# Kernel optimization log

Hardware: AMD Instinct MI355X
Metric: run time of the kernel (lower is better)

Reference implementation:

```python
import jax, jax.numpy as jnp
import numpy as np

N_NODES = 50000


def setup_inputs() -> dict:
    key = jax.random.key(0)
    k1, k2, k3, k4, k5 = jax.random.split(key, 5)
    E = 1600000
    features = jax.random.normal(k1, (N_NODES, 256), dtype=jnp.float32)
    weight = jax.random.normal(k2, (256, 64), dtype=jnp.float32) * (1.0 / np.sqrt(256))
    edge_row = jax.random.randint(k3, (E,), 0, N_NODES, dtype=jnp.int64 if jax.config.jax_enable_x64 else jnp.int32)
    edge_col = jax.random.randint(k4, (E,), 0, N_NODES, dtype=jnp.int64 if jax.config.jax_enable_x64 else jnp.int32)
    edge_weight = jax.random.uniform(k5, (E,), dtype=jnp.float32)
    return {
        "features": features,
        "weight": weight,
        "edge_row": edge_row,
        "edge_col": edge_col,
        "edge_weight": edge_weight,
        "active": 1,
    }


def reference(features, weight, edge_row, edge_col, edge_weight, active):
    # support = features @ W  -- dense projection [N, out]
    support = features @ weight
    # output = spmm(adj, support): gather source rows, scale by edge weight,
    # scatter-add into destination rows (COO SpMM).
    msgs = support[edge_col] * edge_weight[:, None]           # [E, out]
    output = jax.ops.segment_sum(msgs, edge_row, num_segments=N_NODES)  # [N, out]
    if active:
        output = jnp.tanh(output)
    return output
```

## Files before the change

kernel.cpp:

```cpp
#include <hip/hip_runtime.h>
#include <hip/hip_fp16.h>
#include <math.h>

#define N_NODES 50000
#define IN_F 256
#define OUT_F 64
#define NBUCK 512
#define BROWS 98
#define CHUNK 6272
#define NI4   (CHUNK / 4)
#define CAPB 3584

typedef unsigned int uint;
typedef __attribute__((ext_vector_type(8))) short short8v;
typedef __attribute__((ext_vector_type(4))) short short4v;
typedef __attribute__((ext_vector_type(4))) float f32x4;


__device__ __forceinline__ short bf16_trunc(float f) {
    return (short)(__float_as_uint(f) >> 16);
}
__device__ __forceinline__ float bf16_tof(short s) {
    return __uint_as_float(((uint)(unsigned short)s) << 16);
}
__device__ __forceinline__ short bf16_rne(float f) {
    uint u = __float_as_uint(f);
    uint r = u + 0x7FFF + ((u >> 16) & 1);
    return (short)(r >> 16);
}

__global__ __launch_bounds__(256) void wprep_kernel(const float* __restrict__ W,
                                                    short* __restrict__ Whi,
                                                    short* __restrict__ Wlo,
                                                    int* __restrict__ gcnt) {
    const int t = threadIdx.x;
    const int k0 = blockIdx.x * 32;
    if (blockIdx.x == 0) {
        for (int i = t; i < NBUCK; i += 256) gcnt[i] = 0;
    }

    __shared__ float buf[32][65];
    for (int i = t; i < 32 * 64; i += 256) {
        int kk = i >> 6, c = i & 63;
        buf[kk][c] = W[(k0 + kk) * 64 + c];
    }
    __syncthreads();
    {
        int c = t & 63, g = t >> 6;
        short8v vh, vl;
        for (int j = 0; j < 8; ++j) {
            float f = buf[g * 8 + j][c];
            short h = bf16_trunc(f);
            vh[j] = h;
            vl[j] = bf16_rne(f - bf16_tof(h));
        }
        *(short8v*)&Whi[c * IN_F + k0 + g * 8] = vh;
        *(short8v*)&Wlo[c * IN_F + k0 + g * 8] = vl;
    }
}

__global__ __launch_bounds__(256) void gemm_kernel(const float* __restrict__ feat,
                                                   const short* __restrict__ Whi,
                                                   const short* __restrict__ Wlo,
                                                   __half* __restrict__ sup) {
    __shared__ short lds[15360];
    short* As_hi = lds;
    short* As_lo = lds + 5120;
    short* Bs_hi = lds + 10240;
    short* Bs_lo = lds + 12800;

    const int t = threadIdx.x;
    const int row0 = blockIdx.x * 128;
    const int l = t & 63;
    const int lr = l & 15;
    const int lk = (l >> 4) * 8;
    const int wrow = (t >> 6) * 32;

    const int ar = t >> 1, aq = t & 1;
    int gr = row0 + ar; if (gr >= N_NODES) gr = N_NODES - 1;
    const float4* asrc = (const float4*)(feat + (size_t)gr * IN_F);
    const int bc = t >> 2, bp = t & 3;

    f32x4 acc[2][4];
#pragma unroll
    for (int m = 0; m < 2; ++m)
#pragma unroll
        for (int nn = 0; nn < 4; ++nn) acc[m][nn] = (f32x4)(0.f);

    for (int ch = 0; ch < 8; ++ch) {
        float4 av[4];
#pragma unroll
        for (int i = 0; i < 4; ++i) av[i] = asrc[ch * 8 + aq * 4 + i];
        short8v bh = *(const short8v*)(Whi + bc * IN_F + ch * 32 + bp * 8);
        short8v bl = *(const short8v*)(Wlo + bc * IN_F + ch * 32 + bp * 8);

        __syncthreads();
#pragma unroll
        for (int i = 0; i < 4; ++i) {
            float fx[4] = {av[i].x, av[i].y, av[i].z, av[i].w};
            short4v h4, l4;
#pragma unroll
            for (int j = 0; j < 4; ++j) {
                short h = bf16_trunc(fx[j]);
                h4[j] = h;
                l4[j] = bf16_rne(fx[j] - bf16_tof(h));
            }
            *(short4v*)&As_hi[ar * 40 + aq * 16 + i * 4] = h4;
            *(short4v*)&As_lo[ar * 40 + aq * 16 + i * 4] = l4;
        }
        *(short8v*)&Bs_hi[bc * 40 + bp * 8] = bh;
        *(short8v*)&Bs_lo[bc * 40 + bp * 8] = bl;
        __syncthreads();

        short8v ah[2], al[2], wh[4], wl[4];
#pragma unroll
        for (int m = 0; m < 2; ++m) {
            ah[m] = *(short8v*)&As_hi[(wrow + m * 16 + lr) * 40 + lk];
            al[m] = *(short8v*)&As_lo[(wrow + m * 16 + lr) * 40 + lk];
        }
#pragma unroll
        for (int nn = 0; nn < 4; ++nn) {
            wh[nn] = *(short8v*)&Bs_hi[(nn * 16 + lr) * 40 + lk];
            wl[nn] = *(short8v*)&Bs_lo[(nn * 16 + lr) * 40 + lk];
        }
#pragma unroll
        for (int m = 0; m < 2; ++m)
#pragma unroll
            for (int nn = 0; nn < 4; ++nn) {
                acc[m][nn] = __builtin_amdgcn_mfma_f32_16x16x32_bf16(ah[m], wh[nn], acc[m][nn], 0, 0, 0);
                acc[m][nn] = __builtin_amdgcn_mfma_f32_16x16x32_bf16(ah[m], wl[nn], acc[m][nn], 0, 0, 0);
                acc[m][nn] = __builtin_amdgcn_mfma_f32_16x16x32_bf16(al[m], wh[nn], acc[m][nn], 0, 0, 0);
            }
    }

    __syncthreads();
    short* sup_s = lds;
#pragma unroll
    for (int m = 0; m < 2; ++m) {
        int rr = wrow + m * 16 + (l >> 4) * 4;
#pragma unroll
        for (int nn = 0; nn < 4; ++nn) {
            int cc = nn * 16 + lr;
#pragma unroll
            for (int j = 0; j < 4; ++j) {
                __half h = __float2half(acc[m][nn][j]);
                sup_s[(rr + j) * 64 + cc] = *(short*)&h;
            }
        }
    }
    __syncthreads();
    {
        int r = t >> 1, sg = (t & 1) * 32;
        int grow = row0 + r;
        if (grow < N_NODES) {
            const uint4* s4 = (const uint4*)&sup_s[r * 64 + sg];
            uint4* d4 = (uint4*)(sup + (size_t)grow * OUT_F + sg);
            d4[0] = s4[0];
            d4[1] = s4[1];
            d4[2] = s4[2];
            d4[3] = s4[3];
        }
    }
}

__global__ __launch_bounds__(1024) void bin_kernel(const int* __restrict__ erow,
                                                   const int* __restrict__ ecol,
                                                   const float* __restrict__ ew,
                                                   int* __restrict__ gcnt,
                                                   int2* __restrict__ ecw, int E) {
    __shared__ int   h[NBUCK];
    __shared__ uint  pkst[CHUNK];
    __shared__ float wst[CHUNK];
    const int t = threadIdx.x;
    const int base = blockIdx.x * CHUNK;

    for (int i = t; i < NBUCK; i += 1024) h[i] = 0;
    __syncthreads();

    for (int i4 = t; i4 < NI4; i4 += 1024) {
        const int e4 = base + 4 * i4;
        if (e4 + 3 < E) {
            int4   r4 = *(const int4*)(erow + e4);
            int4   c4 = *(const int4*)(ecol + e4);
            float4 w4 = *(const float4*)(ew + e4);
            pkst[4 * i4 + 0] = ((uint)r4.x << 16) | (uint)c4.x;
            pkst[4 * i4 + 1] = ((uint)r4.y << 16) | (uint)c4.y;
            pkst[4 * i4 + 2] = ((uint)r4.z << 16) | (uint)c4.z;
            pkst[4 * i4 + 3] = ((uint)r4.w << 16) | (uint)c4.w;
            *(float4*)(wst + 4 * i4) = w4;
            atomicAdd(&h[(uint)r4.x / BROWS], 1);
            atomicAdd(&h[(uint)r4.y / BROWS], 1);
            atomicAdd(&h[(uint)r4.z / BROWS], 1);
            atomicAdd(&h[(uint)r4.w / BROWS], 1);
        } else {
            for (int k = 0; k < 4; ++k) {
                int e = e4 + k;
                if (e < E) {
                    int row = erow[e];
                    pkst[4 * i4 + k] = ((uint)row << 16) | (uint)ecol[e];
                    wst[4 * i4 + k] = ew[e];
                    atomicAdd(&h[(uint)row / BROWS], 1);
                }
            }
        }
    }
    __syncthreads();

    for (int i = t; i < NBUCK; i += 1024) {
        int c = h[i];
        if (c > 0) h[i] = atomicAdd(&gcnt[i], c);
    }
    __syncthreads();

    const int lim = min(CHUNK, E - base);
    for (int i = t; i < lim; i += 1024) {
        uint  pk = pkst[i];
        float w  = wst[i];
        uint row = pk >> 16;
        uint b   = row / BROWS;
        uint lr  = row - b * BROWS;
        int pos = atomicAdd(&h[b], 1);
        if (pos < CAPB)
            ecw[(size_t)b * CAPB + pos] =
                make_int2((int)((lr << 16) | (pk & 0xFFFF)), __float_as_int(w));
    }
}

__global__ __launch_bounds__(1024) void reduce_kernel(const __half* __restrict__ sup,
                                                      const int* __restrict__ gcnt,
                                                      const int2* __restrict__ ecw,
                                                      const int* __restrict__ active,
                                                      float* __restrict__ out) {
    __shared__ int2 stA[CAPB];
    __shared__ int2 stB[CAPB];
    __shared__ int h[128];
    __shared__ int sc[128];
    __shared__ int cur[128];
    const int t = threadIdx.x;
    const int b = blockIdx.x;

    int n = gcnt[b]; if (n > CAPB) n = CAPB;
    const int2* eptr = ecw + (size_t)b * CAPB;

    if (t < 128) h[t] = 0;
    __syncthreads();

    for (int i = t; i < n; i += 1024) {
        int2 d = eptr[i];
        stA[i] = d;
        atomicAdd(&h[(d.x >> 16) & 127], 1);
    }
    __syncthreads();

    if (t < 128) sc[t] = h[t];
    __syncthreads();
    for (int off = 1; off < 128; off <<= 1) {
        int u = (t < 128 && t >= off) ? sc[t - off] : 0;
        __syncthreads();
        if (t < 128) sc[t] += u;
        __syncthreads();
    }
    if (t < 128) cur[t] = sc[t] - h[t];
    __syncthreads();

    for (int i = t; i < n; i += 1024) {
        int2 d = stA[i];
        int r = (d.x >> 16) & 127;
        int pos = atomicAdd(&cur[r], 1);
        stB[pos] = make_int2(d.x & 0xFFFF, d.y);
    }
    __syncthreads();

    const int wid  = t >> 6;
    const int lane = t & 63;
    const int hl   = lane & 31;
    const bool hi  = lane >= 32;
    const int act  = *active;

    for (int r = wid; r < BROWS; r += 16) {
        int row = b * BROWS + r;
        if (row >= N_NODES) break;
        const int s = sc[r] - h[r];
        const int e = sc[r];
        float ax = 0.f, ay = 0.f;
        int j = s;
        for (; j + 8 <= e; j += 8) {
#pragma unroll
            for (int q = 0; q < 4; ++q) {
                int2 pa = stB[j + 2 * q];
                int2 pb = stB[j + 2 * q + 1];
                int   col = hi ? pb.x : pa.x;
                float w   = __int_as_float(hi ? pb.y : pa.y);
                const __half2* hp = (const __half2*)(sup + ((size_t)col << 6));
                float2 v = __half22float2(hp[hl]);
                ax += w * v.x;
                ay += w * v.y;
            }
        }
        for (; j + 2 <= e; j += 2) {
            int2 pa = stB[j];
            int2 pb = stB[j + 1];
            int   col = hi ? pb.x : pa.x;
            float w   = __int_as_float(hi ? pb.y : pa.y);
            const __half2* hp = (const __half2*)(sup + ((size_t)col << 6));
            float2 v = __half22float2(hp[hl]);
            ax += w * v.x;
            ay += w * v.y;
        }
        if (j < e) {
            int2 pa = stB[j];
            int   col = pa.x;
            float w   = hi ? 0.f : __int_as_float(pa.y);
            const __half2* hp = (const __half2*)(sup + ((size_t)col << 6));
            float2 v = __half22float2(hp[hl]);
            ax += w * v.x;
            ay += w * v.y;
        }

        ax += __shfl_xor(ax, 32, 64);
        ay += __shfl_xor(ay, 32, 64);

        if (!hi) {
            if (act) { ax = tanhf(ax); ay = tanhf(ay); }
            *(float2*)&out[((size_t)row << 6) + 2 * hl] = make_float2(ax, ay);
        }
    }
}

extern "C" void kernel_launch(void* const* d_in, const int* in_sizes, int n_in,
                              void* d_out, int out_size, void* d_ws, size_t ws_size,
                              hipStream_t stream) {
    const float* feat = (const float*)d_in[0];
    const float* W    = (const float*)d_in[1];
    const int*   erow = (const int*)d_in[2];
    const int*   ecol = (const int*)d_in[3];
    const float* ew   = (const float*)d_in[4];
    const int*   act  = (const int*)d_in[5];
    float* out = (float*)d_out;

    const int E = in_sizes[2];
    const int G = (E + CHUNK - 1) / CHUNK;

    char* ws = (char*)d_ws;
    __half* sup  = (__half*)ws; ws += (size_t)N_NODES * OUT_F * 2;
    int2*   ecw  = (int2*)ws;   ws += (size_t)NBUCK * CAPB * 8;
    int*    gcnt = (int*)ws;    ws += ((size_t)NBUCK * 4 + 15) & ~15;
    short*  Whi  = (short*)ws;  ws += (size_t)OUT_F * IN_F * 2;
    short*  Wlo  = (short*)ws;  ws += (size_t)OUT_F * IN_F * 2;

    wprep_kernel<<<8, 256, 0, stream>>>(W, Whi, Wlo, gcnt);
    gemm_kernel<<<(N_NODES + 127) / 128, 256, 0, stream>>>(feat, Whi, Wlo, sup);
    bin_kernel<<<G, 1024, 0, stream>>>(erow, ecol, ew, gcnt, ecw, E);
    reduce_kernel<<<NBUCK, 1024, 0, stream>>>(sup, gcnt, ecw, act, out);
}
```

Measured before the change: 163.0 us.

## Locally sort edges by bucket in LDS before writing binned output

The binning kernel now computes a prefix sum of per-bucket counts, scatters each chunk's edges into bucket-sorted order in shared memory, and then writes them out contiguously per bucket. The goal is to replace scattered global writes with mostly coalesced runs. The chunk size is halved to fit the extra shared arrays, which doubles the block count and the global atomics on bucket counters. It also adds a 512-wide scan with many barriers per block.

```diff
diff --git a/kernel.cpp b/kernel.cpp
--- a/kernel.cpp
+++ b/kernel.cpp
@@ -7,7 +7,7 @@
 #define OUT_F 64
 #define NBUCK 512
 #define BROWS 98
-#define CHUNK 6272
+#define CHUNK 3136
 #define NI4   (CHUNK / 4)
 #define CAPB 3584
 
@@ -168,11 +168,17 @@
                                                    const float* __restrict__ ew,
                                                    int* __restrict__ gcnt,
                                                    int2* __restrict__ ecw, int E) {
-    __shared__ int   h[NBUCK];
     __shared__ uint  pkst[CHUNK];
     __shared__ float wst[CHUNK];
+    __shared__ uint  spk[CHUNK];
+    __shared__ float sw[CHUNK];
+    __shared__ int h[NBUCK];
+    __shared__ int sc[NBUCK];
+    __shared__ int cur[NBUCK];
+    __shared__ int off[NBUCK];
     const int t = threadIdx.x;
     const int base = blockIdx.x * CHUNK;
+    const int lim = min(CHUNK, E - base);
 
     for (int i = t; i < NBUCK; i += 1024) h[i] = 0;
     __syncthreads();
@@ -206,23 +212,40 @@
     }
     __syncthreads();
 
-    for (int i = t; i < NBUCK; i += 1024) {
-        int c = h[i];
-        if (c > 0) h[i] = atomicAdd(&gcnt[i], c);
-    }
-    __syncthreads();
-
-    const int lim = min(CHUNK, E - base);
+    if (t < NBUCK) sc[t] = h[t];
+    __syncthreads();
+    for (int offd = 1; offd < NBUCK; offd <<= 1) {
+        int u = (t < NBUCK && t >= offd) ? sc[t - offd] : 0;
+        __syncthreads();
+        if (t < NBUCK) sc[t] += u;
+        __syncthreads();
+    }
+    if (t < NBUCK) {
+        int start = sc[t] - h[t];
+        cur[t] = start;
+        int c = h[t];
+        if (c > 0) off[t] = atomicAdd(&gcnt[t], c) - start;
+    }
+    __syncthreads();
+
     for (int i = t; i < lim; i += 1024) {
-        uint  pk = pkst[i];
-        float w  = wst[i];
+        uint pk = pkst[i];
         uint row = pk >> 16;
         uint b   = row / BROWS;
         uint lr  = row - b * BROWS;
-        int pos = atomicAdd(&h[b], 1);
-        if (pos < CAPB)
-            ecw[(size_t)b * CAPB + pos] =
-                make_int2((int)((lr << 16) | (pk & 0xFFFF)), __float_as_int(w));
+        int pos = atomicAdd(&cur[b], 1);
+        spk[pos] = (b << 23) | (lr << 16) | (pk & 0xFFFF);
+        sw[pos]  = wst[i];
+    }
+    __syncthreads();
+
+    for (int i = t; i < lim; i += 1024) {
+        uint pk = spk[i];
+        uint b  = pk >> 23;
+        int  wp = off[b] + i;
+        if (wp < CAPB)
+            ecw[(size_t)b * CAPB + wp] =
+                make_int2((int)(pk & 0x7FFFFF), __float_as_int(sw[i]));
     }
 }
 
```

Measured after the change: 164.4 us. No clear change (+0.8%).

## Fuse weight bf16 split into GEMM and prefetch next K-chunk into registers

Applied to the files above, without the earlier changes.

Removes the separate weight-preparation kernel: each GEMM block now loads fp32 W directly and splits it into bf16 hi/lo parts while staging it into LDS. The gcnt zeroing moves into block 0 of the GEMM. The K-loop now prefetches the next chunk's feature and weight values into registers before the MFMA work, so global loads overlap compute. This saves one kernel launch but redoes the W conversion in every block, using scattered 2-byte LDS stores.

```diff
diff --git a/kernel.cpp b/kernel.cpp
--- a/kernel.cpp
+++ b/kernel.cpp
@@ -29,40 +29,14 @@
     return (short)(r >> 16);
 }
 
-__global__ __launch_bounds__(256) void wprep_kernel(const float* __restrict__ W,
-                                                    short* __restrict__ Whi,
-                                                    short* __restrict__ Wlo,
-                                                    int* __restrict__ gcnt) {
-    const int t = threadIdx.x;
-    const int k0 = blockIdx.x * 32;
+__global__ __launch_bounds__(256) void gemm_kernel(const float* __restrict__ feat,
+                                                   const float* __restrict__ W,
+                                                   __half* __restrict__ sup,
+                                                   int* __restrict__ gcnt) {
     if (blockIdx.x == 0) {
-        for (int i = t; i < NBUCK; i += 256) gcnt[i] = 0;
-    }
-
-    __shared__ float buf[32][65];
-    for (int i = t; i < 32 * 64; i += 256) {
-        int kk = i >> 6, c = i & 63;
-        buf[kk][c] = W[(k0 + kk) * 64 + c];
-    }
-    __syncthreads();
-    {
-        int c = t & 63, g = t >> 6;
-        short8v vh, vl;
-        for (int j = 0; j < 8; ++j) {
-            float f = buf[g * 8 + j][c];
-            short h = bf16_trunc(f);
-            vh[j] = h;
-            vl[j] = bf16_rne(f - bf16_tof(h));
-        }
-        *(short8v*)&Whi[c * IN_F + k0 + g * 8] = vh;
-        *(short8v*)&Wlo[c * IN_F + k0 + g * 8] = vl;
-    }
-}
-
-__global__ __launch_bounds__(256) void gemm_kernel(const float* __restrict__ feat,
-                                                   const short* __restrict__ Whi,
-                                                   const short* __restrict__ Wlo,
-                                                   __half* __restrict__ sup) {
+        for (int i = threadIdx.x; i < NBUCK; i += 256) gcnt[i] = 0;
+    }
+
     __shared__ short lds[15360];
     short* As_hi = lds;
     short* As_lo = lds + 5120;
@@ -79,7 +53,8 @@
     const int ar = t >> 1, aq = t & 1;
     int gr = row0 + ar; if (gr >= N_NODES) gr = N_NODES - 1;
     const float4* asrc = (const float4*)(feat + (size_t)gr * IN_F);
-    const int bc = t >> 2, bp = t & 3;
+    const int kk = t >> 3, c0 = (t & 7) * 8;
+    const float4* wsrc = (const float4*)W;
 
     f32x4 acc[2][4];
 #pragma unroll
@@ -87,30 +62,44 @@
 #pragma unroll
         for (int nn = 0; nn < 4; ++nn) acc[m][nn] = (f32x4)(0.f);
 
+    float4 av[4];
+#pragma unroll
+    for (int i = 0; i < 4; ++i) av[i] = asrc[aq * 4 + i];
+    float4 bv0 = wsrc[(kk * 64 + c0) >> 2];
+    float4 bv1 = wsrc[((kk * 64 + c0) >> 2) + 1];
+
     for (int ch = 0; ch < 8; ++ch) {
-        float4 av[4];
-#pragma unroll
-        for (int i = 0; i < 4; ++i) av[i] = asrc[ch * 8 + aq * 4 + i];
-        short8v bh = *(const short8v*)(Whi + bc * IN_F + ch * 32 + bp * 8);
-        short8v bl = *(const short8v*)(Wlo + bc * IN_F + ch * 32 + bp * 8);
-
+        {
+#pragma unroll
+            for (int i = 0; i < 4; ++i) {
+                float fx[4] = {av[i].x, av[i].y, av[i].z, av[i].w};
+                short4v h4, l4;
+#pragma unroll
+                for (int j = 0; j < 4; ++j) {
+                    short h = bf16_trunc(fx[j]);
+                    h4[j] = h;
+                    l4[j] = bf16_rne(fx[j] - bf16_tof(h));
+                }
+                *(short4v*)&As_hi[ar * 40 + aq * 16 + i * 4] = h4;
+                *(short4v*)&As_lo[ar * 40 + aq * 16 + i * 4] = l4;
+            }
+            float bf[8] = {bv0.x, bv0.y, bv0.z, bv0.w, bv1.x, bv1.y, bv1.z, bv1.w};
+#pragma unroll
+            for (int j = 0; j < 8; ++j) {
+                short h = bf16_trunc(bf[j]);
+                Bs_hi[(c0 + j) * 40 + kk] = h;
+                Bs_lo[(c0 + j) * 40 + kk] = bf16_rne(bf[j] - bf16_tof(h));
+            }
+        }
         __syncthreads();
-#pragma unroll
-        for (int i = 0; i < 4; ++i) {
-            float fx[4] = {av[i].x, av[i].y, av[i].z, av[i].w};
-            short4v h4, l4;
-#pragma unroll
-            for (int j = 0; j < 4; ++j) {
-                short h = bf16_trunc(fx[j]);
-                h4[j] = h;
-                l4[j] = bf16_rne(fx[j] - bf16_tof(h));
-            }
-            *(short4v*)&As_hi[ar * 40 + aq * 16 + i * 4] = h4;
-            *(short4v*)&As_lo[ar * 40 + aq * 16 + i * 4] = l4;
-        }
-        *(short8v*)&Bs_hi[bc * 40 + bp * 8] = bh;
-        *(short8v*)&Bs_lo[bc * 40 + bp * 8] = bl;
-        __syncthreads();
+
+        if (ch < 7) {
+#pragma unroll
+            for (int i = 0; i < 4; ++i) av[i] = asrc[(ch + 1) * 8 + aq * 4 + i];
+            int wb = (((ch + 1) * 32 + kk) * 64 + c0) >> 2;
+            bv0 = wsrc[wb];
+            bv1 = wsrc[wb + 1];
+        }
 
         short8v ah[2], al[2], wh[4], wl[4];
 #pragma unroll
@@ -131,9 +120,9 @@
                 acc[m][nn] = __builtin_amdgcn_mfma_f32_16x16x32_bf16(ah[m], wl[nn], acc[m][nn], 0, 0, 0);
                 acc[m][nn] = __builtin_amdgcn_mfma_f32_16x16x32_bf16(al[m], wh[nn], acc[m][nn], 0, 0, 0);
             }
-    }
-
-    __syncthreads();
+        __syncthreads();
+    }
+
     short* sup_s = lds;
 #pragma unroll
     for (int m = 0; m < 2; ++m) {
@@ -345,11 +334,8 @@
     __half* sup  = (__half*)ws; ws += (size_t)N_NODES * OUT_F * 2;
     int2*   ecw  = (int2*)ws;   ws += (size_t)NBUCK * CAPB * 8;
     int*    gcnt = (int*)ws;    ws += ((size_t)NBUCK * 4 + 15) & ~15;
-    short*  Whi  = (short*)ws;  ws += (size_t)OUT_F * IN_F * 2;
-    short*  Wlo  = (short*)ws;  ws += (size_t)OUT_F * IN_F * 2;
-
-    wprep_kernel<<<8, 256, 0, stream>>>(W, Whi, Wlo, gcnt);
-    gemm_kernel<<<(N_NODES + 127) / 128, 256, 0, stream>>>(feat, Whi, Wlo, sup);
+
+    gemm_kernel<<<(N_NODES + 127) / 128, 256, 0, stream>>>(feat, W, sup, gcnt);
     bin_kernel<<<G, 1024, 0, stream>>>(erow, ecol, ew, gcnt, ecw, E);
     reduce_kernel<<<NBUCK, 1024, 0, stream>>>(sup, gcnt, ecw, act, out);
 }
```

Result: no change. 161.7 us (-0.8%).
